# Performance work log

Measured on AMD Instinct MI355X. Metric: run time of the kernel, lower is better.

## Reference

```python
import jax, jax.numpy as jnp
import numpy as np

N_NODES = 100000
N_EDGES = 1600000
D_IN = 128
D_HID = 128
D_OUT = 1
N_GRAPHS = 512


def setup_inputs() -> dict:
    key = jax.random.key(0)
    ks = jax.random.split(key, 12)
    x = jax.random.normal(ks[0], (N_NODES, D_IN), dtype=jnp.float32)
    edge_index = jax.random.randint(ks[1], (2, N_EDGES), 0, N_NODES, dtype=jnp.int32)
    batch = jnp.sort(jax.random.randint(ks[2], (N_NODES,), 0, N_GRAPHS, dtype=jnp.int32))

    def glorot(k, fan_in, fan_out):
        lim = jnp.sqrt(6.0 / (fan_in + fan_out)).astype(jnp.float32)
        return jax.random.uniform(k, (fan_in, fan_out), jnp.float32, -lim, lim)

    W1 = glorot(ks[3], D_IN, D_HID); b1 = jnp.zeros((D_HID,), jnp.float32)
    W2 = glorot(ks[4], D_HID, D_HID); b2 = jnp.zeros((D_HID,), jnp.float32)
    W3 = glorot(ks[5], D_HID, D_HID); b3 = jnp.zeros((D_HID,), jnp.float32)
    Wfc = glorot(ks[6], D_HID, D_OUT); bfc = jnp.zeros((D_OUT,), jnp.float32)
    return {"x": x, "edge_index": edge_index, "batch": batch,
            "W1": W1, "b1": b1, "W2": W2, "b2": b2, "W3": W3, "b3": b3,
            "Wfc": Wfc, "bfc": bfc}


def reference(x, edge_index, batch, W1, b1, W2, b2, W3, b3, Wfc, bfc):
    N = x.shape[0]
    src, dst = edge_index[0], edge_index[1]
    # GCN symmetric normalization with self-loops: deg = in-degree(A) + 1
    deg = jax.ops.segment_sum(jnp.ones_like(dst, dtype=x.dtype), dst, num_segments=N) + 1.0
    dis = jax.lax.rsqrt(deg)                       # deg^{-1/2}, [N]
    enorm = (dis[src] * dis[dst])[:, None]         # per-edge norm, [E,1]
    snorm = (dis * dis)[:, None]                   # self-loop norm, [N,1]

    def gcn_conv(h, W, b):
        h = h @ W                                  # transform first (standard GCNConv)
        agg = jax.ops.segment_sum(h[src] * enorm, dst, num_segments=N)
        return agg + h * snorm + b

    h = jax.nn.relu(gcn_conv(x, W1, b1))           # dropout p=0 (eval): identity
    h = jax.nn.relu(gcn_conv(h, W2, b2))
    h = jax.nn.relu(gcn_conv(h, W3, b3))

    # global_mean_pool over batch segments
    sums = jax.ops.segment_sum(h, batch, num_segments=N_GRAPHS)
    counts = jax.ops.segment_sum(jnp.ones((N, 1), h.dtype), batch, num_segments=N_GRAPHS)
    pooled = sums / jnp.maximum(counts, 1.0)       # [G, D_HID]
    return pooled @ Wfc + bfc                      # [G, 1]
```

## Files before the change

### kernel.cpp

```cpp
#include <hip/hip_runtime.h>

#define D 128
#define CHUNK 4096
#define SPAD 36

typedef unsigned int uint;
typedef unsigned short ushort;
typedef __attribute__((ext_vector_type(8))) short short8;
typedef __attribute__((ext_vector_type(4))) float floatx4;

__device__ __forceinline__ float bf_lo(uint u) { return __uint_as_float(u << 16); }
__device__ __forceinline__ float bf_hi(uint u) { return __uint_as_float(u & 0xffff0000u); }
__device__ __forceinline__ uint f2bf(float f) {
    uint x = __float_as_uint(f);
    return (x + 0x7fffu + ((x >> 16) & 1u)) >> 16;
}

__global__ void setup_kernel(const float* __restrict__ W1, const float* __restrict__ W2,
                             const float* __restrict__ W3, uint* __restrict__ Wt1,
                             uint* __restrict__ Wt2, uint* __restrict__ Wt3,
                             int* __restrict__ cursor, int NB, int CAP) {
    if (blockIdx.x < 96) {
        int gidx = blockIdx.x * 256 + threadIdx.x;
        int w = gidx >> 13, rem = gidx & 8191;
        int n = rem >> 6, kp = rem & 63;
        const float* W = (w == 0) ? W1 : (w == 1) ? W2 : W3;
        uint* Wt = (w == 0) ? Wt1 : (w == 1) ? Wt2 : Wt3;
        Wt[(n << 6) + kp] = f2bf(W[(2 * kp) * 128 + n]) | (f2bf(W[(2 * kp + 1) * 128 + n]) << 16);
    } else {
        int b = threadIdx.x;
        if (b < NB) cursor[b] = b * CAP;
    }
}

__global__ void bin_kernel(const int* __restrict__ src, const int* __restrict__ dst,
                           int* __restrict__ cursor, uint* __restrict__ binned, int E) {
    __shared__ int cnt[256];
    __shared__ int wcur[256];
    int t = threadIdx.x;
    cnt[t] = 0;
    __syncthreads();
    int base = blockIdx.x * CHUNK + t;
    int dv[16]; uint sv[16];
#pragma unroll
    for (int i = 0; i < 16; i++) {
        int e = base + i * 256;
        int d = (e < E) ? dst[e] : -1;
        dv[i] = d;
        sv[i] = (e < E) ? (uint)src[e] : 0u;
        if (d >= 0) atomicAdd(&cnt[d >> 9], 1);
    }
    __syncthreads();
    {
        int c = cnt[t];
        wcur[t] = c ? atomicAdd(&cursor[t], c) : 0;
    }
    __syncthreads();
#pragma unroll
    for (int i = 0; i < 16; i++) {
        int d = dv[i];
        if (d >= 0) {
            int p = atomicAdd(&wcur[d >> 9], 1);
            binned[p] = sv[i] | ((uint)(d & 511) << 17);
        }
    }
}

__launch_bounds__(256)
__global__ void bucket_build_kernel(const uint* __restrict__ binned, const int* __restrict__ cursor,
                                    int* __restrict__ offs, int* __restrict__ oend,
                                    int* __restrict__ csr, float* __restrict__ dis,
                                    int N, int CAP) {
    __shared__ int hist[512];
    __shared__ int tsum[256];
    __shared__ int wcur[512];
    int b = blockIdx.x;
    int t = threadIdx.x;
    int s = b * CAP;
    int e = cursor[b];
    hist[t] = 0; hist[t + 256] = 0;
    __syncthreads();
    for (int i = s + t; i < e; i += 256)
        atomicAdd(&hist[(binned[i] >> 17) & 511], 1);
    __syncthreads();
    int h0 = t * 2;
    int v0 = hist[h0], v1 = hist[h0 + 1];
    int ts = v0 + v1;
    tsum[t] = ts;
    __syncthreads();
    for (int off = 1; off < 256; off <<= 1) {
        int x = (t >= off) ? tsum[t - off] : 0;
        __syncthreads();
        tsum[t] += x;
        __syncthreads();
    }
    int excl = tsum[t] - ts;
    int o0 = excl, o1 = o0 + v0;
    int n0 = (b << 9) + h0;
    wcur[h0] = s + o0; wcur[h0 + 1] = s + o1;
    if (n0 < N)     { offs[n0]     = s + o0; oend[n0]     = s + o0 + v0; dis[n0]     = rsqrtf((float)v0 + 1.0f); }
    if (n0 + 1 < N) { offs[n0 + 1] = s + o1; oend[n0 + 1] = s + o1 + v1; dis[n0 + 1] = rsqrtf((float)v1 + 1.0f); }
    __syncthreads();
    for (int i = s + t; i < e; i += 256) {
        uint en = binned[i];
        int local = (en >> 17) & 511;
        int p = atomicAdd(&wcur[local], 1);
        csr[p] = (int)(en & 0x1ffffu);
    }
}

template <bool F32A>
__launch_bounds__(256)
__global__ void gemm_mfma_kernel(const void* __restrict__ Aptr, const uint* __restrict__ Wt,
                                 const float* __restrict__ dis, uint* __restrict__ U, int N) {
    __shared__ uint lds[128 * SPAD * 2];
    uint* a_lds = lds;
    uint* w_lds = lds + 128 * SPAD;
    int tid = threadIdx.x;
    int m0 = blockIdx.x * 128;
    int wave = tid >> 6, lane = tid & 63;
    int lm = lane & 15, quad = lane >> 4;

    floatx4 acc[2][8];
#pragma unroll
    for (int i = 0; i < 2; i++)
#pragma unroll
        for (int j = 0; j < 8; j++)
            acc[i][j] = (floatx4){0.f, 0.f, 0.f, 0.f};

    if (F32A) {
        const float* Af = (const float*)Aptr;
#pragma unroll
        for (int i = 0; i < 8; i++) {
            int gi = tid + i * 256;
            int row = gi >> 4, j = gi & 15;
            int grow = m0 + row;
            float4 v = (grow < N) ? *(const float4*)&Af[(size_t)grow * 128 + j * 4]
                                  : make_float4(0.f, 0.f, 0.f, 0.f);
            uint2 o;
            o.x = f2bf(v.x) | (f2bf(v.y) << 16);
            o.y = f2bf(v.z) | (f2bf(v.w) << 16);
            *(uint2*)&a_lds[row * SPAD + j * 2] = o;
        }
    } else {
        const uint* Ab = (const uint*)Aptr;
#pragma unroll
        for (int i = 0; i < 4; i++) {
            int gi = tid + i * 256;
            int row = gi >> 3, c4 = (gi & 7) << 2;
            int grow = m0 + row;
            uint4 av = (grow < N) ? *(const uint4*)&Ab[(size_t)grow * 64 + c4]
                                  : make_uint4(0u, 0u, 0u, 0u);
            *(uint4*)&a_lds[row * SPAD + c4] = av;
        }
    }
#pragma unroll
    for (int i = 0; i < 4; i++) {
        int gi = tid + i * 256;
        int row = gi >> 3, c4 = (gi & 7) << 2;
        *(uint4*)&w_lds[row * SPAD + c4] = *(const uint4*)&Wt[(size_t)row * 64 + c4];
    }
    __syncthreads();

    float4 pf_f[8];
    uint4 pf_u[4];
    if (F32A) {
        const float* Af = (const float*)Aptr;
#pragma unroll
        for (int i = 0; i < 8; i++) {
            int gi = tid + i * 256;
            int row = gi >> 4, j = gi & 15;
            int grow = m0 + row;
            pf_f[i] = (grow < N) ? *(const float4*)&Af[(size_t)grow * 128 + 64 + j * 4]
                                 : make_float4(0.f, 0.f, 0.f, 0.f);
        }
    } else {
        const uint* Ab = (const uint*)Aptr;
#pragma unroll
        for (int i = 0; i < 4; i++) {
            int gi = tid + i * 256;
            int row = gi >> 3, c4 = (gi & 7) << 2;
            int grow = m0 + row;
            pf_u[i] = (grow < N) ? *(const uint4*)&Ab[(size_t)grow * 64 + 32 + c4]
                                 : make_uint4(0u, 0u, 0u, 0u);
        }
    }

#pragma unroll
    for (int kc = 0; kc < 2; kc++) {
        int ko = kc * 16 + quad * 4;
        short8 b[8];
#pragma unroll
        for (int nt = 0; nt < 8; nt++)
            b[nt] = *(short8*)&w_lds[(nt * 16 + lm) * SPAD + ko];
        short8 a0 = *(short8*)&a_lds[(wave * 32 + lm) * SPAD + ko];
        short8 a1 = *(short8*)&a_lds[(wave * 32 + 16 + lm) * SPAD + ko];
#pragma unroll
        for (int nt = 0; nt < 8; nt++) {
            acc[0][nt] = __builtin_amdgcn_mfma_f32_16x16x32_bf16(a0, b[nt], acc[0][nt], 0, 0, 0);
            acc[1][nt] = __builtin_amdgcn_mfma_f32_16x16x32_bf16(a1, b[nt], acc[1][nt], 0, 0, 0);
        }
    }
    __syncthreads();

    if (F32A) {
#pragma unroll
        for (int i = 0; i < 8; i++) {
            int gi = tid + i * 256;
            int row = gi >> 4, j = gi & 15;
            uint2 o;
            o.x = f2bf(pf_f[i].x) | (f2bf(pf_f[i].y) << 16);
            o.y = f2bf(pf_f[i].z) | (f2bf(pf_f[i].w) << 16);
            *(uint2*)&a_lds[row * SPAD + j * 2] = o;
        }
    } else {
#pragma unroll
        for (int i = 0; i < 4; i++) {
            int gi = tid + i * 256;
            int row = gi >> 3, c4 = (gi & 7) << 2;
            *(uint4*)&a_lds[row * SPAD + c4] = pf_u[i];
        }
    }
#pragma unroll
    for (int i = 0; i < 4; i++) {
        int gi = tid + i * 256;
        int row = gi >> 3, c4 = (gi & 7) << 2;
        *(uint4*)&w_lds[row * SPAD + c4] = *(const uint4*)&Wt[(size_t)row * 64 + 32 + c4];
    }
    __syncthreads();

#pragma unroll
    for (int kc = 0; kc < 2; kc++) {
        int ko = kc * 16 + quad * 4;
        short8 b[8];
#pragma unroll
        for (int nt = 0; nt < 8; nt++)
            b[nt] = *(short8*)&w_lds[(nt * 16 + lm) * SPAD + ko];
        short8 a0 = *(short8*)&a_lds[(wave * 32 + lm) * SPAD + ko];
        short8 a1 = *(short8*)&a_lds[(wave * 32 + 16 + lm) * SPAD + ko];
#pragma unroll
        for (int nt = 0; nt < 8; nt++) {
            acc[0][nt] = __builtin_amdgcn_mfma_f32_16x16x32_bf16(a0, b[nt], acc[0][nt], 0, 0, 0);
            acc[1][nt] = __builtin_amdgcn_mfma_f32_16x16x32_bf16(a1, b[nt], acc[1][nt], 0, 0, 0);
        }
    }
    __syncthreads();

    ushort* o_lds = (ushort*)lds;
    float dv[2][4];
#pragma unroll
    for (int ms = 0; ms < 2; ms++)
#pragma unroll
        for (int r = 0; r < 4; r++) {
            int row = m0 + wave * 32 + ms * 16 + quad * 4 + r;
            dv[ms][r] = (row < N) ? dis[row] : 0.f;
        }
#pragma unroll
    for (int ms = 0; ms < 2; ms++)
#pragma unroll
        for (int nt = 0; nt < 8; nt++)
#pragma unroll
            for (int r = 0; r < 4; r++) {
                int row = wave * 32 + ms * 16 + quad * 4 + r;
                int col = nt * 16 + lm;
                o_lds[row * 132 + col] = (ushort)f2bf(acc[ms][nt][r] * dv[ms][r]);
            }
    __syncthreads();
#pragma unroll
    for (int i = 0; i < 16; i++) {
        int gi = tid + i * 256;
        int row = gi >> 5, c2 = gi & 31;
        int grow = m0 + row;
        if (grow < N) {
            uint2 v = *(uint2*)&lds[row * 66 + c2 * 2];
            *(uint2*)&U[(size_t)grow * 64 + c2 * 2] = v;
        }
    }
}

__launch_bounds__(256)
__global__ void aggregate_kernel(const uint* __restrict__ U, const int* __restrict__ offs,
                                 const int* __restrict__ oend, const int* __restrict__ csr_src,
                                 const float* __restrict__ dis, const float* __restrict__ bias,
                                 uint* __restrict__ H, int N) {
    int wave = threadIdx.x >> 6;
    int lane = threadIdx.x & 63;
    int n = blockIdx.x * 4 + wave;
    if (n >= N) return;
    int g = lane >> 4, i16 = lane & 15;

    float a0 = 0.f, a1 = 0.f, a2 = 0.f, a3 = 0.f, a4 = 0.f, a5 = 0.f, a6 = 0.f, a7 = 0.f;
    int s = offs[n], e = oend[n];
    int j = s + g;
    for (; j + 12 < e; j += 16) {
        int s0 = csr_src[j], s1 = csr_src[j + 4], s2 = csr_src[j + 8], s3 = csr_src[j + 12];
        uint4 u0 = *(const uint4*)&U[(size_t)s0 * 64 + i16 * 4];
        uint4 u1 = *(const uint4*)&U[(size_t)s1 * 64 + i16 * 4];
        uint4 u2 = *(const uint4*)&U[(size_t)s2 * 64 + i16 * 4];
        uint4 u3 = *(const uint4*)&U[(size_t)s3 * 64 + i16 * 4];
        a0 += bf_lo(u0.x) + bf_lo(u1.x) + bf_lo(u2.x) + bf_lo(u3.x);
        a1 += bf_hi(u0.x) + bf_hi(u1.x) + bf_hi(u2.x) + bf_hi(u3.x);
        a2 += bf_lo(u0.y) + bf_lo(u1.y) + bf_lo(u2.y) + bf_lo(u3.y);
        a3 += bf_hi(u0.y) + bf_hi(u1.y) + bf_hi(u2.y) + bf_hi(u3.y);
        a4 += bf_lo(u0.z) + bf_lo(u1.z) + bf_lo(u2.z) + bf_lo(u3.z);
        a5 += bf_hi(u0.z) + bf_hi(u1.z) + bf_hi(u2.z) + bf_hi(u3.z);
        a6 += bf_lo(u0.w) + bf_lo(u1.w) + bf_lo(u2.w) + bf_lo(u3.w);
        a7 += bf_hi(u0.w) + bf_hi(u1.w) + bf_hi(u2.w) + bf_hi(u3.w);
    }
    for (; j < e; j += 4) {
        int s0 = csr_src[j];
        uint4 u = *(const uint4*)&U[(size_t)s0 * 64 + i16 * 4];
        a0 += bf_lo(u.x); a1 += bf_hi(u.x);
        a2 += bf_lo(u.y); a3 += bf_hi(u.y);
        a4 += bf_lo(u.z); a5 += bf_hi(u.z);
        a6 += bf_lo(u.w); a7 += bf_hi(u.w);
    }
    a0 += __shfl_xor(a0, 16); a0 += __shfl_xor(a0, 32);
    a1 += __shfl_xor(a1, 16); a1 += __shfl_xor(a1, 32);
    a2 += __shfl_xor(a2, 16); a2 += __shfl_xor(a2, 32);
    a3 += __shfl_xor(a3, 16); a3 += __shfl_xor(a3, 32);
    a4 += __shfl_xor(a4, 16); a4 += __shfl_xor(a4, 32);
    a5 += __shfl_xor(a5, 16); a5 += __shfl_xor(a5, 32);
    a6 += __shfl_xor(a6, 16); a6 += __shfl_xor(a6, 32);
    a7 += __shfl_xor(a7, 16); a7 += __shfl_xor(a7, 32);

    if (g == 0) {
        uint4 su = *(const uint4*)&U[(size_t)n * 64 + i16 * 4];
        a0 += bf_lo(su.x); a1 += bf_hi(su.x);
        a2 += bf_lo(su.y); a3 += bf_hi(su.y);
        a4 += bf_lo(su.z); a5 += bf_hi(su.z);
        a6 += bf_lo(su.w); a7 += bf_hi(su.w);
        float dn = dis[n];
        float4 b0 = *(const float4*)&bias[i16 * 8];
        float4 b1 = *(const float4*)&bias[i16 * 8 + 4];
        uint4 o;
        o.x = f2bf(fmaxf(fmaf(a0, dn, b0.x), 0.f)) | (f2bf(fmaxf(fmaf(a1, dn, b0.y), 0.f)) << 16);
        o.y = f2bf(fmaxf(fmaf(a2, dn, b0.z), 0.f)) | (f2bf(fmaxf(fmaf(a3, dn, b0.w), 0.f)) << 16);
        o.z = f2bf(fmaxf(fmaf(a4, dn, b1.x), 0.f)) | (f2bf(fmaxf(fmaf(a5, dn, b1.y), 0.f)) << 16);
        o.w = f2bf(fmaxf(fmaf(a6, dn, b1.z), 0.f)) | (f2bf(fmaxf(fmaf(a7, dn, b1.w), 0.f)) << 16);
        *(uint4*)&H[(size_t)n * 64 + i16 * 4] = o;
    }
}

__launch_bounds__(512)
__global__ void pool_fc_kernel(const uint* __restrict__ H, const int* __restrict__ batch,
                               const float* __restrict__ Wfc, const float* __restrict__ bfc,
                               float* __restrict__ out, int N) {
    __shared__ float2 red[512];
    int g = blockIdx.x;
    int t = threadIdx.x;
    int rid = t >> 6, lane = t & 63;

    int lo = 0, hi = N;
    while (lo < hi) { int mid = (lo + hi) >> 1; if (batch[mid] < g) lo = mid + 1; else hi = mid; }
    int st = lo;
    hi = N;
    while (lo < hi) { int mid = (lo + hi) >> 1; if (batch[mid] < g + 1) lo = mid + 1; else hi = mid; }
    int en = lo;

    float ax = 0.f, ay = 0.f;
    for (int r = st + rid; r < en; r += 8) {
        uint u = H[(size_t)r * 64 + lane];
        ax += bf_lo(u);
        ay += bf_hi(u);
    }
    red[t] = make_float2(ax, ay);
    __syncthreads();
    if (rid == 0) {
        float2 sv = red[lane];
#pragma unroll
        for (int i = 1; i < 8; i++) { sv.x += red[i * 64 + lane].x; sv.y += red[i * 64 + lane].y; }
        float cnt = fmaxf((float)(en - st), 1.0f);
        float p = (sv.x / cnt) * Wfc[lane * 2] + (sv.y / cnt) * Wfc[lane * 2 + 1];
        for (int off = 32; off > 0; off >>= 1) p += __shfl_down(p, off);
        if (lane == 0) out[g] = p + bfc[0];
    }
}

extern "C" void kernel_launch(void* const* d_in, const int* in_sizes, int n_in,
                              void* d_out, int out_size, void* d_ws, size_t ws_size,
                              hipStream_t stream) {
    const float* x   = (const float*)d_in[0];
    const int* eidx  = (const int*)d_in[1];
    const int* batch = (const int*)d_in[2];
    const float* W1  = (const float*)d_in[3];
    const float* b1  = (const float*)d_in[4];
    const float* W2  = (const float*)d_in[5];
    const float* b2  = (const float*)d_in[6];
    const float* W3  = (const float*)d_in[7];
    const float* b3  = (const float*)d_in[8];
    const float* Wfc = (const float*)d_in[9];
    const float* bfc = (const float*)d_in[10];
    float* out = (float*)d_out;

    int N = in_sizes[2];
    int E = in_sizes[1] / 2;
    int G = out_size;
    int NB = (N + 511) >> 9;
    int CAP = E / NB + 1536;

    const int* src = eidx;
    const int* dst = eidx + E;

    char* ws = (char*)d_ws;
    size_t off = 0;
    auto alloc = [&](size_t bytes) -> void* {
        void* p = ws + off;
        off += (bytes + 255) & ~(size_t)255;
        return p;
    };
    size_t winsz = (size_t)NB * CAP;
    uint* Ua     = (uint*)alloc((size_t)N * 64 * sizeof(uint));
    uint* Ub     = (uint*)alloc((size_t)N * 64 * sizeof(uint));
    uint* Wt1    = (uint*)alloc(8192 * sizeof(uint));
    uint* Wt2    = (uint*)alloc(8192 * sizeof(uint));
    uint* Wt3    = (uint*)alloc(8192 * sizeof(uint));
    float* dis   = (float*)alloc((size_t)N * sizeof(float));
    int* offs    = (int*)alloc((size_t)N * sizeof(int));
    int* oend    = (int*)alloc((size_t)N * sizeof(int));
    int* csr     = (int*)alloc(winsz * sizeof(int));
    uint* binned = (uint*)alloc(winsz * sizeof(uint));
    int* cursor  = (int*)alloc(256 * sizeof(int));
    (void)ws_size; (void)n_in;

    int cb = (E + CHUNK - 1) / CHUNK;

    setup_kernel<<<97, 256, 0, stream>>>(W1, W2, W3, Wt1, Wt2, Wt3, cursor, NB, CAP);
    bin_kernel<<<cb, 256, 0, stream>>>(src, dst, cursor, binned, E);
    bucket_build_kernel<<<NB, 256, 0, stream>>>(binned, cursor, offs, oend, csr, dis, N, CAP);

    int gb = (N + 127) / 128;
    int ab = (N + 3) / 4;

    gemm_mfma_kernel<true><<<gb, 256, 0, stream>>>(x, Wt1, dis, Ua, N);
    aggregate_kernel<<<ab, 256, 0, stream>>>(Ua, offs, oend, csr, dis, b1, Ub, N);
    gemm_mfma_kernel<false><<<gb, 256, 0, stream>>>(Ub, Wt2, dis, Ua, N);
    aggregate_kernel<<<ab, 256, 0, stream>>>(Ua, offs, oend, csr, dis, b2, Ub, N);
    gemm_mfma_kernel<false><<<gb, 256, 0, stream>>>(Ub, Wt3, dis, Ua, N);
    aggregate_kernel<<<ab, 256, 0, stream>>>(Ua, offs, oend, csr, dis, b3, Ub, N);
    pool_fc_kernel<<<G, 512, 0, stream>>>(Ub, batch, Wfc, bfc, out, N);
}
```

Baseline: 406.8 us.

## Fuse last aggregation with mean-pool via atomics and halve binning chunk size

The final GCN aggregation now accumulates ReLU outputs straight into a per-graph pooled buffer with float atomics, so the last-layer H is never written to memory and read back. A small fc kernel then divides by the node counts and applies the output linear layer. Separately, the edge-binning chunk is halved to give more blocks and fewer registers per thread. Atomics on 512 graph rows cause contention, since sorted batch ids put neighbouring nodes into the same graph, and summation order becomes nondeterministic. An extra memset launch is also added.

```diff
diff --git a/kernel.cpp b/kernel.cpp
--- a/kernel.cpp
+++ b/kernel.cpp
@@ -1,7 +1,7 @@
 #include <hip/hip_runtime.h>
 
 #define D 128
-#define CHUNK 4096
+#define CHUNK 2048
 #define SPAD 36
 
 typedef unsigned int uint;
@@ -41,9 +41,9 @@
     cnt[t] = 0;
     __syncthreads();
     int base = blockIdx.x * CHUNK + t;
-    int dv[16]; uint sv[16];
-#pragma unroll
-    for (int i = 0; i < 16; i++) {
+    int dv[8]; uint sv[8];
+#pragma unroll
+    for (int i = 0; i < 8; i++) {
         int e = base + i * 256;
         int d = (e < E) ? dst[e] : -1;
         dv[i] = d;
@@ -57,7 +57,7 @@
     }
     __syncthreads();
 #pragma unroll
-    for (int i = 0; i < 16; i++) {
+    for (int i = 0; i < 8; i++) {
         int d = dv[i];
         if (d >= 0) {
             int p = atomicAdd(&wcur[d >> 9], 1);
@@ -342,14 +342,85 @@
     }
 }
 
-__launch_bounds__(512)
-__global__ void pool_fc_kernel(const uint* __restrict__ H, const int* __restrict__ batch,
-                               const float* __restrict__ Wfc, const float* __restrict__ bfc,
-                               float* __restrict__ out, int N) {
-    __shared__ float2 red[512];
+__launch_bounds__(256)
+__global__ void aggregate_pool_kernel(const uint* __restrict__ U, const int* __restrict__ offs,
+                                      const int* __restrict__ oend, const int* __restrict__ csr_src,
+                                      const float* __restrict__ dis, const float* __restrict__ bias,
+                                      const int* __restrict__ batch, float* __restrict__ pooled,
+                                      int N) {
+    int wave = threadIdx.x >> 6;
+    int lane = threadIdx.x & 63;
+    int n = blockIdx.x * 4 + wave;
+    if (n >= N) return;
+    int g = lane >> 4, i16 = lane & 15;
+
+    float a0 = 0.f, a1 = 0.f, a2 = 0.f, a3 = 0.f, a4 = 0.f, a5 = 0.f, a6 = 0.f, a7 = 0.f;
+    int s = offs[n], e = oend[n];
+    int j = s + g;
+    for (; j + 12 < e; j += 16) {
+        int s0 = csr_src[j], s1 = csr_src[j + 4], s2 = csr_src[j + 8], s3 = csr_src[j + 12];
+        uint4 u0 = *(const uint4*)&U[(size_t)s0 * 64 + i16 * 4];
+        uint4 u1 = *(const uint4*)&U[(size_t)s1 * 64 + i16 * 4];
+        uint4 u2 = *(const uint4*)&U[(size_t)s2 * 64 + i16 * 4];
+        uint4 u3 = *(const uint4*)&U[(size_t)s3 * 64 + i16 * 4];
+        a0 += bf_lo(u0.x) + bf_lo(u1.x) + bf_lo(u2.x) + bf_lo(u3.x);
+        a1 += bf_hi(u0.x) + bf_hi(u1.x) + bf_hi(u2.x) + bf_hi(u3.x);
+        a2 += bf_lo(u0.y) + bf_lo(u1.y) + bf_lo(u2.y) + bf_lo(u3.y);
+        a3 += bf_hi(u0.y) + bf_hi(u1.y) + bf_hi(u2.y) + bf_hi(u3.y);
+        a4 += bf_lo(u0.z) + bf_lo(u1.z) + bf_lo(u2.z) + bf_lo(u3.z);
+        a5 += bf_hi(u0.z) + bf_hi(u1.z) + bf_hi(u2.z) + bf_hi(u3.z);
+        a6 += bf_lo(u0.w) + bf_lo(u1.w) + bf_lo(u2.w) + bf_lo(u3.w);
+        a7 += bf_hi(u0.w) + bf_hi(u1.w) + bf_hi(u2.w) + bf_hi(u3.w);
+    }
+    for (; j < e; j += 4) {
+        int s0 = csr_src[j];
+        uint4 u = *(const uint4*)&U[(size_t)s0 * 64 + i16 * 4];
+        a0 += bf_lo(u.x); a1 += bf_hi(u.x);
+        a2 += bf_lo(u.y); a3 += bf_hi(u.y);
+        a4 += bf_lo(u.z); a5 += bf_hi(u.z);
+        a6 += bf_lo(u.w); a7 += bf_hi(u.w);
+    }
+    a0 += __shfl_xor(a0, 16); a0 += __shfl_xor(a0, 32);
+    a1 += __shfl_xor(a1, 16); a1 += __shfl_xor(a1, 32);
+    a2 += __shfl_xor(a2, 16); a2 += __shfl_xor(a2, 32);
+    a3 += __shfl_xor(a3, 16); a3 += __shfl_xor(a3, 32);
+    a4 += __shfl_xor(a4, 16); a4 += __shfl_xor(a4, 32);
+    a5 += __shfl_xor(a5, 16); a5 += __shfl_xor(a5, 32);
+    a6 += __shfl_xor(a6, 16); a6 += __shfl_xor(a6, 32);
+    a7 += __shfl_xor(a7, 16); a7 += __shfl_xor(a7, 32);
+
+    if (g == 0) {
+        uint4 su = *(const uint4*)&U[(size_t)n * 64 + i16 * 4];
+        a0 += bf_lo(su.x); a1 += bf_hi(su.x);
+        a2 += bf_lo(su.y); a3 += bf_hi(su.y);
+        a4 += bf_lo(su.z); a5 += bf_hi(su.z);
+        a6 += bf_lo(su.w); a7 += bf_hi(su.w);
+        float dn = dis[n];
+        float4 b0 = *(const float4*)&bias[i16 * 8];
+        float4 b1 = *(const float4*)&bias[i16 * 8 + 4];
+        float h0 = fmaxf(fmaf(a0, dn, b0.x), 0.f);
+        float h1 = fmaxf(fmaf(a1, dn, b0.y), 0.f);
+        float h2 = fmaxf(fmaf(a2, dn, b0.z), 0.f);
+        float h3 = fmaxf(fmaf(a3, dn, b0.w), 0.f);
+        float h4 = fmaxf(fmaf(a4, dn, b1.x), 0.f);
+        float h5 = fmaxf(fmaf(a5, dn, b1.y), 0.f);
+        float h6 = fmaxf(fmaf(a6, dn, b1.z), 0.f);
+        float h7 = fmaxf(fmaf(a7, dn, b1.w), 0.f);
+        float* pp = &pooled[(size_t)batch[n] * 128 + i16 * 8];
+        atomicAdd(pp + 0, h0); atomicAdd(pp + 1, h1);
+        atomicAdd(pp + 2, h2); atomicAdd(pp + 3, h3);
+        atomicAdd(pp + 4, h4); atomicAdd(pp + 5, h5);
+        atomicAdd(pp + 6, h6); atomicAdd(pp + 7, h7);
+    }
+}
+
+__launch_bounds__(128)
+__global__ void fc_kernel(const float* __restrict__ pooled, const int* __restrict__ batch,
+                          const float* __restrict__ Wfc, const float* __restrict__ bfc,
+                          float* __restrict__ out, int N) {
+    __shared__ float red[2];
     int g = blockIdx.x;
-    int t = threadIdx.x;
-    int rid = t >> 6, lane = t & 63;
+    int c = threadIdx.x;
 
     int lo = 0, hi = N;
     while (lo < hi) { int mid = (lo + hi) >> 1; if (batch[mid] < g) lo = mid + 1; else hi = mid; }
@@ -358,23 +429,12 @@
     while (lo < hi) { int mid = (lo + hi) >> 1; if (batch[mid] < g + 1) lo = mid + 1; else hi = mid; }
     int en = lo;
 
-    float ax = 0.f, ay = 0.f;
-    for (int r = st + rid; r < en; r += 8) {
-        uint u = H[(size_t)r * 64 + lane];
-        ax += bf_lo(u);
-        ay += bf_hi(u);
-    }
-    red[t] = make_float2(ax, ay);
-    __syncthreads();
-    if (rid == 0) {
-        float2 sv = red[lane];
-#pragma unroll
-        for (int i = 1; i < 8; i++) { sv.x += red[i * 64 + lane].x; sv.y += red[i * 64 + lane].y; }
-        float cnt = fmaxf((float)(en - st), 1.0f);
-        float p = (sv.x / cnt) * Wfc[lane * 2] + (sv.y / cnt) * Wfc[lane * 2 + 1];
-        for (int off = 32; off > 0; off >>= 1) p += __shfl_down(p, off);
-        if (lane == 0) out[g] = p + bfc[0];
-    }
+    float cnt = fmaxf((float)(en - st), 1.0f);
+    float p = (pooled[(size_t)g * 128 + c] / cnt) * Wfc[c];
+    for (int off = 32; off > 0; off >>= 1) p += __shfl_down(p, off);
+    if ((c & 63) == 0) red[c >> 6] = p;
+    __syncthreads();
+    if (c == 0) out[g] = red[0] + red[1] + bfc[0];
 }
 
 extern "C" void kernel_launch(void* const* d_in, const int* in_sizes, int n_in,
@@ -421,7 +481,10 @@
     int* csr     = (int*)alloc(winsz * sizeof(int));
     uint* binned = (uint*)alloc(winsz * sizeof(uint));
     int* cursor  = (int*)alloc(256 * sizeof(int));
+    float* pooled = (float*)alloc((size_t)G * 128 * sizeof(float));
     (void)ws_size; (void)n_in;
+
+    hipMemsetAsync(pooled, 0, (size_t)G * 128 * sizeof(float), stream);
 
     int cb = (E + CHUNK - 1) / CHUNK;
 
@@ -437,6 +500,6 @@
     gemm_mfma_kernel<false><<<gb, 256, 0, stream>>>(Ub, Wt2, dis, Ua, N);
     aggregate_kernel<<<ab, 256, 0, stream>>>(Ua, offs, oend, csr, dis, b2, Ub, N);
     gemm_mfma_kernel<false><<<gb, 256, 0, stream>>>(Ub, Wt3, dis, Ua, N);
-    aggregate_kernel<<<ab, 256, 0, stream>>>(Ua, offs, oend, csr, dis, b3, Ub, N);
-    pool_fc_kernel<<<G, 512, 0, stream>>>(Ub, batch, Wfc, bfc, out, N);
-}
+    aggregate_pool_kernel<<<ab, 256, 0, stream>>>(Ua, offs, oend, csr, dis, b3, batch, pooled, N);
+    fc_kernel<<<G, 128, 0, stream>>>(pooled, batch, Wfc, bfc, out, N);
+}
```

Result: slower. 833.7 us (+104.9%).
